# Kernel tuning notes

Measured on AMD Instinct MI355X. Metric: run time of the kernel, lower is better.

Reference implementation:

```python
import jax, jax.numpy as jnp
import numpy as np


def setup_inputs() -> dict:
    key = jax.random.key(0)
    k1, k2 = jax.random.split(key)
    B, P, H, W, D, C = 4, 8, 32, 32, 32, 16
    input_fmap = jax.random.normal(k1, (B, P, H, W, D, C), dtype=jnp.float32)
    # theta ~ identity affine (rows act on [y, x, z, 1]) + small noise so most
    # sampled coordinates fall inside the volume
    base = jnp.concatenate([jnp.eye(3, dtype=jnp.float32), jnp.zeros((3, 1), jnp.float32)], axis=1)
    theta = base[None, None] + 0.1 * jax.random.normal(k2, (B, P, 3, 4), dtype=jnp.float32)
    return {"input_fmap": input_fmap, "theta": theta}


def reference(input_fmap, theta):
    B, P, H, W, D, C = input_fmap.shape
    # --- affine grid generation (matches tf.meshgrid 'xy' indexing) ---
    xs = jnp.arange(W, dtype=jnp.float32)
    ys = jnp.arange(H, dtype=jnp.float32)
    zs = jnp.arange(D, dtype=jnp.float32)
    x_t, y_t, z_t = jnp.meshgrid(xs, ys, zs, indexing="xy")  # each (H, W, D)
    grid = jnp.stack([y_t.ravel(), x_t.ravel(), z_t.ravel(),
                      jnp.ones(H * W * D, jnp.float32)], axis=0)  # (4, HWD)
    batch_grids = jnp.einsum("bpij,jn->bpin", theta, grid)  # (B, P, 3, HWD)
    batch_grids = batch_grids.reshape(B, P, 3, H, W, D)
    y_s = batch_grids[:, :, 0]
    x_s = batch_grids[:, :, 1]
    z_s = batch_grids[:, :, 2]

    # --- trilinear sampling on a 2-voxel zero-padded volume ---
    fmap_p = jnp.pad(input_fmap, ((0, 0), (0, 0), (2, 2), (2, 2), (2, 2), (0, 0)))
    x = x_s + 2.0
    y = y_s + 2.0
    z = z_s + 2.0
    # NOTE: original code clips all three axes with H + 2 (faithful reproduction)
    hi = H + 2
    x0 = jnp.clip(jnp.floor(x).astype(jnp.int32), 0, hi)
    y0 = jnp.clip(jnp.floor(y).astype(jnp.int32), 0, hi)
    z0 = jnp.clip(jnp.floor(z).astype(jnp.int32), 0, hi)
    x1, y1, z1 = x0 + 1, y0 + 1, z0 + 1

    b_idx = jnp.arange(B)[:, None, None, None, None]
    p_idx = jnp.arange(P)[None, :, None, None, None]

    def gather(yy, xx, zz):
        # indices stacked as [y, x, z] in the original -> axes (H_pad, W_pad, D_pad)
        return fmap_p[b_idx, p_idx, yy, xx, zz]  # (B, P, H, W, D, C)

    c000 = gather(y0, x0, z0)
    c001 = gather(y0, x0, z1)
    c010 = gather(y1, x0, z0)
    c011 = gather(y1, x0, z1)
    c100 = gather(y0, x1, z0)
    c101 = gather(y0, x1, z1)
    c110 = gather(y1, x1, z0)
    c111 = gather(y1, x1, z1)

    xd = (x - x0.astype(jnp.float32))[..., None]
    yd = (y - y0.astype(jnp.float32))[..., None]
    zd = (z - z0.astype(jnp.float32))[..., None]

    out = (c000 * (1 - xd) * (1 - yd) * (1 - zd)
           + c100 * xd * (1 - yd) * (1 - zd)
           + c010 * (1 - xd) * yd * (1 - zd)
           + c001 * (1 - xd) * (1 - yd) * zd
           + c101 * xd * (1 - yd) * zd
           + c011 * (1 - xd) * yd * zd
           + c110 * xd * yd * (1 - zd)
           + c111 * xd * yd * zd)
    return out
```

## Files before the change

### kernel.cpp

```cpp
#include <hip/hip_runtime.h>

constexpr int B = 4, P = 8, H = 32, W = 32, D = 32, C = 16;

using f32x4 = __attribute__((ext_vector_type(4))) float;

__global__ __launch_bounds__(256) void resample3d_kernel(
    const float* __restrict__ fmap,
    const float* __restrict__ theta,
    float* __restrict__ out)
{
    const int bp  = blockIdx.x >> 9;
    const int tid = threadIdx.x;
    const int c4  = tid & 3;
    const int vox = blockIdx.x * 64 + (tid >> 2);
    const int k   =  vox        & (D - 1);
    const int j   = (vox >> 5)  & (W - 1);
    const int i   = (vox >> 10) & (H - 1);

    const float4* th4 = (const float4*)(theta + bp * 12);
    const float4 t0 = th4[0];
    const float4 t1 = th4[1];
    const float4 t2 = th4[2];

    const float fi = (float)i, fj = (float)j, fk = (float)k;
    const float y = fmaf(t0.x, fi, fmaf(t0.y, fj, fmaf(t0.z, fk, t0.w))) + 2.0f;
    const float x = fmaf(t1.x, fi, fmaf(t1.y, fj, fmaf(t1.z, fk, t1.w))) + 2.0f;
    const float z = fmaf(t2.x, fi, fmaf(t2.y, fj, fmaf(t2.z, fk, t2.w))) + 2.0f;

    const float fy0 = fminf(fmaxf(floorf(y), 0.0f), 34.0f);
    const float fx0 = fminf(fmaxf(floorf(x), 0.0f), 34.0f);
    const float fz0 = fminf(fmaxf(floorf(z), 0.0f), 34.0f);
    const float yd = y - fy0, xd = x - fx0, zd = z - fz0;

    const int ty0 = (int)fy0 - 2, tx0 = (int)fx0 - 2, tz0 = (int)fz0 - 2;

    float wy[2], wx[2], wz[2];
    int   iy[2], ix[2], iz[2];
    wy[0] = ((unsigned)ty0       < (unsigned)H) ? (1.0f - yd) : 0.0f;
    wy[1] = ((unsigned)(ty0 + 1) < (unsigned)H) ? yd          : 0.0f;
    wx[0] = ((unsigned)tx0       < (unsigned)W) ? (1.0f - xd) : 0.0f;
    wx[1] = ((unsigned)(tx0 + 1) < (unsigned)W) ? xd          : 0.0f;
    wz[0] = ((unsigned)tz0       < (unsigned)D) ? (1.0f - zd) : 0.0f;
    wz[1] = ((unsigned)(tz0 + 1) < (unsigned)D) ? zd          : 0.0f;
    iy[0] = min(max(ty0, 0), H - 1);  iy[1] = min(max(ty0 + 1, 0), H - 1);
    ix[0] = min(max(tx0, 0), W - 1);  ix[1] = min(max(tx0 + 1, 0), W - 1);
    iz[0] = min(max(tz0, 0), D - 1);  iz[1] = min(max(tz0 + 1, 0), D - 1);

    const float* base = fmap + bp * (H * W * D * C) + c4 * 4;

    f32x4 acc = {0.f, 0.f, 0.f, 0.f};
    #pragma unroll
    for (int a = 0; a < 2; ++a) {
        const int offy = iy[a] * (W * D * C);
        #pragma unroll
        for (int b2 = 0; b2 < 2; ++b2) {
            const int offyx = offy + ix[b2] * (D * C);
            const float wyx = wy[a] * wx[b2];
            #pragma unroll
            for (int c2 = 0; c2 < 2; ++c2) {
                const float w = wyx * wz[c2];
                const f32x4 v = *(const f32x4*)(base + offyx + iz[c2] * C);
                acc += w * v;
            }
        }
    }

    *(f32x4*)(out + vox * C + c4 * 4) = acc;
}

extern "C" void kernel_launch(void* const* d_in, const int* in_sizes, int n_in,
                              void* d_out, int out_size, void* d_ws, size_t ws_size,
                              hipStream_t stream) {
    const float* fmap  = (const float*)d_in[0];
    const float* theta = (const float*)d_in[1];
    float* out = (float*)d_out;

    const int total_threads = B * P * H * W * D * 4;
    const int block = 256;
    const int grid = total_threads / block;
    resample3d_kernel<<<grid, block, 0, stream>>>(fmap, theta, out);
}
```

Measured before the change: 29.14 us.

## Split z-corners across thread pairs, remap blocks across XCDs, nontemporal stores

Doubles the thread count so each pair of threads handles the two z-corners of a voxel. Each thread issues 4 gathers instead of 8, and the pair reduces its results with a cross-lane shuffle. Blocks are remapped so consecutive launch indices interleave across 8 groups, likely to spread each batch-patch volume across XCD L2 caches, and outputs use nontemporal stores. The cost is twice the index and weight arithmetic, the extra shuffles, and half the lanes staying idle at the store.

After: 29.71 us. Within noise of the previous version (+2.0%).

```diff
diff --git a/kernel.cpp b/kernel.cpp
--- a/kernel.cpp
+++ b/kernel.cpp
@@ -9,13 +9,17 @@
     const float* __restrict__ theta,
     float* __restrict__ out)
 {
-    const int bp  = blockIdx.x >> 9;
-    const int tid = threadIdx.x;
-    const int c4  = tid & 3;
-    const int vox = blockIdx.x * 64 + (tid >> 2);
+    const int orig = blockIdx.x;
+    const int virt = (orig & 7) * 4096 + (orig >> 3);
+
+    const int tid  = threadIdx.x;
+    const int zbit = (tid >> 2) & 1;
+    const int chunk = tid & 3;
+    const int vox = virt * 32 + (tid >> 3);
     const int k   =  vox        & (D - 1);
     const int j   = (vox >> 5)  & (W - 1);
     const int i   = (vox >> 10) & (H - 1);
+    const int bp  = virt >> 10;
 
     const float4* th4 = (const float4*)(theta + bp * 12);
     const float4 t0 = th4[0];
@@ -31,41 +35,48 @@
     const float fx0 = fminf(fmaxf(floorf(x), 0.0f), 34.0f);
     const float fz0 = fminf(fmaxf(floorf(z), 0.0f), 34.0f);
     const float yd = y - fy0, xd = x - fx0, zd = z - fz0;
-
     const int ty0 = (int)fy0 - 2, tx0 = (int)fx0 - 2, tz0 = (int)fz0 - 2;
 
-    float wy[2], wx[2], wz[2];
-    int   iy[2], ix[2], iz[2];
+    float wy[2], wx[2];
+    int   iy[2], ix[2];
     wy[0] = ((unsigned)ty0       < (unsigned)H) ? (1.0f - yd) : 0.0f;
     wy[1] = ((unsigned)(ty0 + 1) < (unsigned)H) ? yd          : 0.0f;
     wx[0] = ((unsigned)tx0       < (unsigned)W) ? (1.0f - xd) : 0.0f;
     wx[1] = ((unsigned)(tx0 + 1) < (unsigned)W) ? xd          : 0.0f;
-    wz[0] = ((unsigned)tz0       < (unsigned)D) ? (1.0f - zd) : 0.0f;
-    wz[1] = ((unsigned)(tz0 + 1) < (unsigned)D) ? zd          : 0.0f;
     iy[0] = min(max(ty0, 0), H - 1);  iy[1] = min(max(ty0 + 1, 0), H - 1);
     ix[0] = min(max(tx0, 0), W - 1);  ix[1] = min(max(tx0 + 1, 0), W - 1);
-    iz[0] = min(max(tz0, 0), D - 1);  iz[1] = min(max(tz0 + 1, 0), D - 1);
 
-    const float* base = fmap + bp * (H * W * D * C) + c4 * 4;
+    const int tz = tz0 + zbit;
+    const float wzl = ((unsigned)tz < (unsigned)D)
+                        ? (zbit ? zd : (1.0f - zd)) : 0.0f;
+    const int izl = min(max(tz, 0), D - 1);
+
+    const float* base = fmap + bp * (H * W * D * C) + izl * C + chunk * 4;
+
+    f32x4 v[4];
+    float w[4];
+    #pragma unroll
+    for (int a = 0; a < 2; ++a)
+        #pragma unroll
+        for (int b2 = 0; b2 < 2; ++b2) {
+            const int cn = a * 2 + b2;
+            w[cn] = wy[a] * wx[b2] * wzl;
+            v[cn] = *(const f32x4*)(base + iy[a] * (W * D * C) + ix[b2] * (D * C));
+        }
 
     f32x4 acc = {0.f, 0.f, 0.f, 0.f};
     #pragma unroll
-    for (int a = 0; a < 2; ++a) {
-        const int offy = iy[a] * (W * D * C);
-        #pragma unroll
-        for (int b2 = 0; b2 < 2; ++b2) {
-            const int offyx = offy + ix[b2] * (D * C);
-            const float wyx = wy[a] * wx[b2];
-            #pragma unroll
-            for (int c2 = 0; c2 < 2; ++c2) {
-                const float w = wyx * wz[c2];
-                const f32x4 v = *(const f32x4*)(base + offyx + iz[c2] * C);
-                acc += w * v;
-            }
-        }
+    for (int cn = 0; cn < 4; ++cn)
+        acc += w[cn] * v[cn];
+
+    #pragma unroll
+    for (int r = 0; r < 4; ++r)
+        acc[r] += __shfl_xor(acc[r], 4);
+
+    if (!zbit) {
+        float* outp = out + (size_t)vox * C + chunk * 4;
+        __builtin_nontemporal_store(acc, (f32x4*)outp);
     }
-
-    *(f32x4*)(out + vox * C + c4 * 4) = acc;
 }
 
 extern "C" void kernel_launch(void* const* d_in, const int* in_sizes, int n_in,
@@ -75,7 +86,7 @@
     const float* theta = (const float*)d_in[1];
     float* out = (float*)d_out;
 
-    const int total_threads = B * P * H * W * D * 4;
+    const int total_threads = B * P * H * W * D * 8;
     const int block = 256;
     const int grid = total_threads / block;
     resample3d_kernel<<<grid, block, 0, stream>>>(fmap, theta, out);
```

## Convert feature map to fp16 in workspace and gather with one thread per voxel

Applied to the files above, without the earlier changes.

Adds a pre-pass kernel that converts the fp32 input volume to fp16 in the workspace. A new gather kernel then reads the eight corners as half-precision vectors, one thread per voxel covering all 16 channels, and accumulates in fp16 before widening to fp32. It also swizzles block order across batch/patch volumes and uses nontemporal stores. The intent is to halve the bytes moved by the random gathers, at the cost of an extra full read and write pass over the input and reduced accuracy from fp16 weights and accumulation.

Result: slower. 66.13 us (+126.9%).

```diff
diff --git a/kernel.cpp b/kernel.cpp
--- a/kernel.cpp
+++ b/kernel.cpp
@@ -3,19 +3,33 @@
 constexpr int B = 4, P = 8, H = 32, W = 32, D = 32, C = 16;
 
 using f32x4 = __attribute__((ext_vector_type(4))) float;
+using f16x8 = __attribute__((ext_vector_type(8))) _Float16;
 
-__global__ __launch_bounds__(256) void resample3d_kernel(
-    const float* __restrict__ fmap,
+__global__ __launch_bounds__(256) void cvt_kernel(const float* __restrict__ in,
+                                                  _Float16* __restrict__ o) {
+    const int t = blockIdx.x * 256 + threadIdx.x;
+    const f32x4* p = (const f32x4*)in + (size_t)t * 2;
+    const f32x4 a = p[0], b = p[1];
+    f16x8 h;
+    h[0] = (_Float16)a[0]; h[1] = (_Float16)a[1];
+    h[2] = (_Float16)a[2]; h[3] = (_Float16)a[3];
+    h[4] = (_Float16)b[0]; h[5] = (_Float16)b[1];
+    h[6] = (_Float16)b[2]; h[7] = (_Float16)b[3];
+    *((f16x8*)o + t) = h;
+}
+
+__global__ __launch_bounds__(256) void gather_kernel(
+    const _Float16* __restrict__ fmap16,
     const float* __restrict__ theta,
     float* __restrict__ out)
 {
-    const int bp  = blockIdx.x >> 9;
-    const int tid = threadIdx.x;
-    const int c4  = tid & 3;
-    const int vox = blockIdx.x * 64 + (tid >> 2);
-    const int k   =  vox        & (D - 1);
-    const int j   = (vox >> 5)  & (W - 1);
-    const int i   = (vox >> 10) & (H - 1);
+    const int orig = blockIdx.x;
+    const int virt = (orig & 7) * 512 + (orig >> 3);
+    const int vox  = virt * 256 + threadIdx.x;
+    const int k = vox & (D - 1);
+    const int j = (vox >> 5) & (W - 1);
+    const int i = (vox >> 10) & (H - 1);
+    const int bp = vox >> 15;
 
     const float4* th4 = (const float4*)(theta + bp * 12);
     const float4 t0 = th4[0];
@@ -31,7 +45,94 @@
     const float fx0 = fminf(fmaxf(floorf(x), 0.0f), 34.0f);
     const float fz0 = fminf(fmaxf(floorf(z), 0.0f), 34.0f);
     const float yd = y - fy0, xd = x - fx0, zd = z - fz0;
+    const int ty0 = (int)fy0 - 2, tx0 = (int)fx0 - 2, tz0 = (int)fz0 - 2;
 
+    float wy[2], wx[2], wz[2];
+    int   iy[2], ix[2], iz[2];
+    wy[0] = ((unsigned)ty0       < (unsigned)H) ? (1.0f - yd) : 0.0f;
+    wy[1] = ((unsigned)(ty0 + 1) < (unsigned)H) ? yd          : 0.0f;
+    wx[0] = ((unsigned)tx0       < (unsigned)W) ? (1.0f - xd) : 0.0f;
+    wx[1] = ((unsigned)(tx0 + 1) < (unsigned)W) ? xd          : 0.0f;
+    wz[0] = ((unsigned)tz0       < (unsigned)D) ? (1.0f - zd) : 0.0f;
+    wz[1] = ((unsigned)(tz0 + 1) < (unsigned)D) ? zd          : 0.0f;
+    iy[0] = min(max(ty0, 0), H - 1);  iy[1] = min(max(ty0 + 1, 0), H - 1);
+    ix[0] = min(max(tx0, 0), W - 1);  ix[1] = min(max(tx0 + 1, 0), W - 1);
+    iz[0] = min(max(tz0, 0), D - 1);  iz[1] = min(max(tz0 + 1, 0), D - 1);
+
+    int   off[8];
+    float w[8];
+    #pragma unroll
+    for (int a = 0; a < 2; ++a)
+        #pragma unroll
+        for (int b2 = 0; b2 < 2; ++b2)
+            #pragma unroll
+            for (int c2 = 0; c2 < 2; ++c2) {
+                const int cn = a * 4 + b2 * 2 + c2;
+                off[cn] = ((iy[a] * W + ix[b2]) * D + iz[c2]) * C;
+                w[cn]   = wy[a] * wx[b2] * wz[c2];
+            }
+
+    const _Float16* base = fmap16 + (size_t)bp * (H * W * D * C);
+
+    f16x8 v0[8], v1[8];
+    #pragma unroll
+    for (int cn = 0; cn < 8; ++cn) {
+        v0[cn] = *(const f16x8*)(base + off[cn]);
+        v1[cn] = *(const f16x8*)(base + off[cn] + 8);
+    }
+
+    f16x8 aA0 = 0, aA1 = 0, aB0 = 0, aB1 = 0;
+    #pragma unroll
+    for (int cn = 0; cn < 4; ++cn) {
+        const _Float16 hw = (_Float16)w[cn];
+        aA0 += hw * v0[cn];
+        aA1 += hw * v1[cn];
+    }
+    #pragma unroll
+    for (int cn = 4; cn < 8; ++cn) {
+        const _Float16 hw = (_Float16)w[cn];
+        aB0 += hw * v0[cn];
+        aB1 += hw * v1[cn];
+    }
+
+    float r[16];
+    #pragma unroll
+    for (int c = 0; c < 8; ++c) {
+        r[c]     = (float)aA0[c] + (float)aB0[c];
+        r[c + 8] = (float)aA1[c] + (float)aB1[c];
+    }
+
+    float* op = out + (size_t)vox * C;
+    __builtin_nontemporal_store(*(f32x4*)&r[0],  (f32x4*)op);
+    __builtin_nontemporal_store(*(f32x4*)&r[4],  (f32x4*)(op + 4));
+    __builtin_nontemporal_store(*(f32x4*)&r[8],  (f32x4*)(op + 8));
+    __builtin_nontemporal_store(*(f32x4*)&r[12], (f32x4*)(op + 12));
+}
+
+__global__ __launch_bounds__(256) void fallback_kernel(
+    const float* __restrict__ fmap, const float* __restrict__ theta,
+    float* __restrict__ out)
+{
+    const int bp  = blockIdx.x >> 9;
+    const int tid = threadIdx.x;
+    const int c4  = tid & 3;
+    const int vox = blockIdx.x * 64 + (tid >> 2);
+    const int k   =  vox        & (D - 1);
+    const int j   = (vox >> 5)  & (W - 1);
+    const int i   = (vox >> 10) & (H - 1);
+
+    const float4* th4 = (const float4*)(theta + bp * 12);
+    const float4 t0 = th4[0], t1 = th4[1], t2 = th4[2];
+
+    const float fi = (float)i, fj = (float)j, fk = (float)k;
+    const float y = fmaf(t0.x, fi, fmaf(t0.y, fj, fmaf(t0.z, fk, t0.w))) + 2.0f;
+    const float x = fmaf(t1.x, fi, fmaf(t1.y, fj, fmaf(t1.z, fk, t1.w))) + 2.0f;
+    const float z = fmaf(t2.x, fi, fmaf(t2.y, fj, fmaf(t2.z, fk, t2.w))) + 2.0f;
+
+    const float fy0 = fminf(fmaxf(floorf(y), 0.0f), 34.0f);
+    const float fx0 = fminf(fmaxf(floorf(x), 0.0f), 34.0f);
+    const float fz0 = fminf(fmaxf(floorf(z), 0.0f), 34.0f);
+    const float yd = y - fy0, xd = x - fx0, zd = z - fz0;
     const int ty0 = (int)fy0 - 2, tx0 = (int)fx0 - 2, tz0 = (int)fz0 - 2;
 
     float wy[2], wx[2], wz[2];
@@ -47,25 +148,19 @@
     iz[0] = min(max(tz0, 0), D - 1);  iz[1] = min(max(tz0 + 1, 0), D - 1);
 
     const float* base = fmap + bp * (H * W * D * C) + c4 * 4;
-
     f32x4 acc = {0.f, 0.f, 0.f, 0.f};
     #pragma unroll
-    for (int a = 0; a < 2; ++a) {
-        const int offy = iy[a] * (W * D * C);
+    for (int a = 0; a < 2; ++a)
         #pragma unroll
-        for (int b2 = 0; b2 < 2; ++b2) {
-            const int offyx = offy + ix[b2] * (D * C);
-            const float wyx = wy[a] * wx[b2];
+        for (int b2 = 0; b2 < 2; ++b2)
             #pragma unroll
             for (int c2 = 0; c2 < 2; ++c2) {
-                const float w = wyx * wz[c2];
-                const f32x4 v = *(const f32x4*)(base + offyx + iz[c2] * C);
-                acc += w * v;
+                const float wgt = wy[a] * wx[b2] * wz[c2];
+                const f32x4 v = *(const f32x4*)(
+                    base + ((iy[a] * W + ix[b2]) * D + iz[c2]) * C);
+                acc += wgt * v;
             }
-        }
-    }
-
-    *(f32x4*)(out + vox * C + c4 * 4) = acc;
+    *(f32x4*)(out + (size_t)vox * C + c4 * 4) = acc;
 }
 
 extern "C" void kernel_launch(void* const* d_in, const int* in_sizes, int n_in,
@@ -75,8 +170,15 @@
     const float* theta = (const float*)d_in[1];
     float* out = (float*)d_out;
 
-    const int total_threads = B * P * H * W * D * 4;
-    const int block = 256;
-    const int grid = total_threads / block;
-    resample3d_kernel<<<grid, block, 0, stream>>>(fmap, theta, out);
+    const size_t need = (size_t)(B * P * H * W * D * C) * sizeof(_Float16);
+    if (ws_size >= need) {
+        _Float16* f16buf = (_Float16*)d_ws;
+        const int cvt_blocks = (B * P * H * W * D * C / 8) / 256;
+        cvt_kernel<<<cvt_blocks, 256, 0, stream>>>(fmap, f16buf);
+        const int gat_blocks = (B * P * H * W * D) / 256;
+        gather_kernel<<<gat_blocks, 256, 0, stream>>>(f16buf, theta, out);
+    } else {
+        const int total_threads = B * P * H * W * D * 4;
+        fallback_kernel<<<total_threads / 256, 256, 0, stream>>>(fmap, theta, out);
+    }
 }
```

## Stage per-tile source bounding box in LDS as fp16 and interpolate from shared memory

Applied to the files above, without the earlier changes.

Each block now handles an 8x8x8 output tile. It computes the affine bounding box of the source voxels the tile needs and, when that box fits in capacity, loads the box into LDS converted to fp16. The eight trilinear taps are then read from shared memory and accumulated with packed fp16 math. Blocks are also remapped so that neighbouring block IDs cover different tiles, and a global-memory fp32 fallback remains for large boxes. The aim is to cut redundant global gathers, at the cost of fp16 precision loss in both the staged values and the accumulation, plus extra LDS use that limits occupancy.

Result: slower. 59.01 us (+102.5%).

```diff
diff --git a/kernel.cpp b/kernel.cpp
--- a/kernel.cpp
+++ b/kernel.cpp
@@ -2,70 +2,178 @@
 
 constexpr int B = 4, P = 8, H = 32, W = 32, D = 32, C = 16;
 
+constexpr int TI = 8, TJ = 8, TK = 8;
+constexpr int TILE_VOX = TI * TJ * TK;
+constexpr int CAP = 2048;
+
 using f32x4 = __attribute__((ext_vector_type(4))) float;
+using f16x4 = __attribute__((ext_vector_type(4))) _Float16;
+using f16x8 = __attribute__((ext_vector_type(8))) _Float16;
 
-__global__ __launch_bounds__(256) void resample3d_kernel(
+__global__ __launch_bounds__(256) void resample_tile(
     const float* __restrict__ fmap,
     const float* __restrict__ theta,
     float* __restrict__ out)
 {
-    const int bp  = blockIdx.x >> 9;
-    const int tid = threadIdx.x;
-    const int c4  = tid & 3;
-    const int vox = blockIdx.x * 64 + (tid >> 2);
-    const int k   =  vox        & (D - 1);
-    const int j   = (vox >> 5)  & (W - 1);
-    const int i   = (vox >> 10) & (H - 1);
+    extern __shared__ _Float16 sm[];
+
+    const int orig = blockIdx.x;
+    const int virt = (orig & 7) * 256 + (orig >> 3);
+    const int bp = virt >> 6;
+    const int t6 = virt & 63;
+    const int i0 = (t6 >> 4) * TI;
+    const int j0 = ((t6 >> 2) & 3) * TJ;
+    const int k0 = (t6 & 3) * TK;
 
     const float4* th4 = (const float4*)(theta + bp * 12);
     const float4 t0 = th4[0];
     const float4 t1 = th4[1];
     const float4 t2 = th4[2];
 
-    const float fi = (float)i, fj = (float)j, fk = (float)k;
-    const float y = fmaf(t0.x, fi, fmaf(t0.y, fj, fmaf(t0.z, fk, t0.w))) + 2.0f;
-    const float x = fmaf(t1.x, fi, fmaf(t1.y, fj, fmaf(t1.z, fk, t1.w))) + 2.0f;
-    const float z = fmaf(t2.x, fi, fmaf(t2.y, fj, fmaf(t2.z, fk, t2.w))) + 2.0f;
+    const float fi0 = (float)i0, fj0 = (float)j0, fk0 = (float)k0;
+    const float pyb = fmaf(t0.x, fi0, fmaf(t0.y, fj0, fmaf(t0.z, fk0, t0.w))) + 2.0f;
+    const float pxb = fmaf(t1.x, fi0, fmaf(t1.y, fj0, fmaf(t1.z, fk0, t1.w))) + 2.0f;
+    const float pzb = fmaf(t2.x, fi0, fmaf(t2.y, fj0, fmaf(t2.z, fk0, t2.w))) + 2.0f;
 
-    const float fy0 = fminf(fmaxf(floorf(y), 0.0f), 34.0f);
-    const float fx0 = fminf(fmaxf(floorf(x), 0.0f), 34.0f);
-    const float fz0 = fminf(fmaxf(floorf(z), 0.0f), 34.0f);
-    const float yd = y - fy0, xd = x - fx0, zd = z - fz0;
+    const float eyi = t0.x * (TI - 1), eyj = t0.y * (TJ - 1), eyk = t0.z * (TK - 1);
+    const float exi = t1.x * (TI - 1), exj = t1.y * (TJ - 1), exk = t1.z * (TK - 1);
+    const float ezi = t2.x * (TI - 1), ezj = t2.y * (TJ - 1), ezk = t2.z * (TK - 1);
 
-    const int ty0 = (int)fy0 - 2, tx0 = (int)fx0 - 2, tz0 = (int)fz0 - 2;
+    const float pymin = pyb + fminf(eyi, 0.f) + fminf(eyj, 0.f) + fminf(eyk, 0.f);
+    const float pymax = pyb + fmaxf(eyi, 0.f) + fmaxf(eyj, 0.f) + fmaxf(eyk, 0.f);
+    const float pxmin = pxb + fminf(exi, 0.f) + fminf(exj, 0.f) + fminf(exk, 0.f);
+    const float pxmax = pxb + fmaxf(exi, 0.f) + fmaxf(exj, 0.f) + fmaxf(exk, 0.f);
+    const float pzmin = pzb + fminf(ezi, 0.f) + fminf(ezj, 0.f) + fminf(ezk, 0.f);
+    const float pzmax = pzb + fmaxf(ezi, 0.f) + fmaxf(ezj, 0.f) + fmaxf(ezk, 0.f);
 
-    float wy[2], wx[2], wz[2];
-    int   iy[2], ix[2], iz[2];
-    wy[0] = ((unsigned)ty0       < (unsigned)H) ? (1.0f - yd) : 0.0f;
-    wy[1] = ((unsigned)(ty0 + 1) < (unsigned)H) ? yd          : 0.0f;
-    wx[0] = ((unsigned)tx0       < (unsigned)W) ? (1.0f - xd) : 0.0f;
-    wx[1] = ((unsigned)(tx0 + 1) < (unsigned)W) ? xd          : 0.0f;
-    wz[0] = ((unsigned)tz0       < (unsigned)D) ? (1.0f - zd) : 0.0f;
-    wz[1] = ((unsigned)(tz0 + 1) < (unsigned)D) ? zd          : 0.0f;
-    iy[0] = min(max(ty0, 0), H - 1);  iy[1] = min(max(ty0 + 1, 0), H - 1);
-    ix[0] = min(max(tx0, 0), W - 1);  ix[1] = min(max(tx0 + 1, 0), W - 1);
-    iz[0] = min(max(tz0, 0), D - 1);  iz[1] = min(max(tz0 + 1, 0), D - 1);
+    const int tylo = max(0, min((int)fminf(fmaxf(floorf(pymin), 0.f), 34.f) - 2, 31));
+    int       tyhi = min(31, (int)fminf(fmaxf(floorf(pymax), 0.f), 34.f) - 1);
+    tyhi = max(tyhi, tylo);
+    const int txlo = max(0, min((int)fminf(fmaxf(floorf(pxmin), 0.f), 34.f) - 2, 31));
+    int       txhi = min(31, (int)fminf(fmaxf(floorf(pxmax), 0.f), 34.f) - 1);
+    txhi = max(txhi, txlo);
+    const int tzlo = max(0, min((int)fminf(fmaxf(floorf(pzmin), 0.f), 34.f) - 2, 31));
+    int       tzhi = min(31, (int)fminf(fmaxf(floorf(pzmax), 0.f), 34.f) - 1);
+    tzhi = max(tzhi, tzlo);
 
-    const float* base = fmap + bp * (H * W * D * C) + c4 * 4;
+    const int dy = tyhi - tylo + 1;
+    const int dx = txhi - txlo + 1;
+    const int dz = tzhi - tzlo + 1;
+    const int vol = dy * dx * dz;
+    const bool fast = (vol <= CAP);
 
-    f32x4 acc = {0.f, 0.f, 0.f, 0.f};
-    #pragma unroll
-    for (int a = 0; a < 2; ++a) {
-        const int offy = iy[a] * (W * D * C);
-        #pragma unroll
-        for (int b2 = 0; b2 < 2; ++b2) {
-            const int offyx = offy + ix[b2] * (D * C);
-            const float wyx = wy[a] * wx[b2];
-            #pragma unroll
-            for (int c2 = 0; c2 < 2; ++c2) {
-                const float w = wyx * wz[c2];
-                const f32x4 v = *(const f32x4*)(base + offyx + iz[c2] * C);
-                acc += w * v;
+    const float* slice = fmap + bp * (H * W * D * C);
+
+    if (fast) {
+        const int wv = threadIdx.x >> 6;
+        const int ln = threadIdx.x & 63;
+        const int rowch = dz * 4;
+        int ry = 0, rx = wv;
+        while (rx >= dx) { rx -= dx; ++ry; }
+        while (ry < dy) {
+            const float* g = slice + ((tylo + ry) * W + (txlo + rx)) * (D * C)
+                                   + tzlo * C;
+            _Float16* l = sm + ((ry * dx + rx) * dz) * 16;
+            for (int cz = ln; cz < rowch; cz += 64) {
+                const f32x4 v = *(const f32x4*)(g + cz * 4);
+                f16x4 h;
+                h[0] = (_Float16)v[0]; h[1] = (_Float16)v[1];
+                h[2] = (_Float16)v[2]; h[3] = (_Float16)v[3];
+                *(f16x4*)(l + cz * 4) = h;
             }
+            rx += 4;
+            while (rx >= dx) { rx -= dx; ++ry; }
         }
     }
+    __syncthreads();
 
-    *(f32x4*)(out + vox * C + c4 * 4) = acc;
+    for (int v = threadIdx.x; v < TILE_VOX; v += 256) {
+        const int li = v >> 6;
+        const int lj = (v >> 3) & 7;
+        const int lk = v & 7;
+        const float fi = (float)(i0 + li), fj = (float)(j0 + lj), fk = (float)(k0 + lk);
+
+        const float py = fmaf(t0.x, fi, fmaf(t0.y, fj, fmaf(t0.z, fk, t0.w))) + 2.0f;
+        const float px = fmaf(t1.x, fi, fmaf(t1.y, fj, fmaf(t1.z, fk, t1.w))) + 2.0f;
+        const float pz = fmaf(t2.x, fi, fmaf(t2.y, fj, fmaf(t2.z, fk, t2.w))) + 2.0f;
+
+        const float fy0 = fminf(fmaxf(floorf(py), 0.f), 34.f);
+        const float fx0 = fminf(fmaxf(floorf(px), 0.f), 34.f);
+        const float fz0 = fminf(fmaxf(floorf(pz), 0.f), 34.f);
+        const float yd = py - fy0, xd = px - fx0, zd = pz - fz0;
+        const int ty0 = (int)fy0 - 2, tx0 = (int)fx0 - 2, tz0 = (int)fz0 - 2;
+
+        float wy[2], wx[2], wz[2];
+        int   iy[2], ix[2], iz[2];
+        wy[0] = ((unsigned)ty0       < (unsigned)H) ? (1.0f - yd) : 0.0f;
+        wy[1] = ((unsigned)(ty0 + 1) < (unsigned)H) ? yd          : 0.0f;
+        wx[0] = ((unsigned)tx0       < (unsigned)W) ? (1.0f - xd) : 0.0f;
+        wx[1] = ((unsigned)(tx0 + 1) < (unsigned)W) ? xd          : 0.0f;
+        wz[0] = ((unsigned)tz0       < (unsigned)D) ? (1.0f - zd) : 0.0f;
+        wz[1] = ((unsigned)(tz0 + 1) < (unsigned)D) ? zd          : 0.0f;
+        iy[0] = min(max(ty0, 0), H - 1);  iy[1] = min(max(ty0 + 1, 0), H - 1);
+        ix[0] = min(max(tx0, 0), W - 1);  ix[1] = min(max(tx0 + 1, 0), W - 1);
+        iz[0] = min(max(tz0, 0), D - 1);  iz[1] = min(max(tz0 + 1, 0), D - 1);
+
+        f32x4 r0, r1, r2, r3;
+
+        if (fast) {
+            int ly[2], lx[2], lz[2];
+            ly[0] = min(max(iy[0] - tylo, 0), dy - 1);
+            ly[1] = min(max(iy[1] - tylo, 0), dy - 1);
+            lx[0] = min(max(ix[0] - txlo, 0), dx - 1);
+            lx[1] = min(max(ix[1] - txlo, 0), dx - 1);
+            lz[0] = min(max(iz[0] - tzlo, 0), dz - 1);
+            lz[1] = min(max(iz[1] - tzlo, 0), dz - 1);
+
+            f16x8 aA0 = 0, aA1 = 0, aB0 = 0, aB1 = 0;
+            #pragma unroll
+            for (int a = 0; a < 2; ++a)
+                #pragma unroll
+                for (int b2 = 0; b2 < 2; ++b2)
+                    #pragma unroll
+                    for (int c2 = 0; c2 < 2; ++c2) {
+                        const int cn = a * 4 + b2 * 2 + c2;
+                        const int vx = ((ly[a] * dx + lx[b2]) * dz + lz[c2]) * 16;
+                        const f16x8 lo = *(const f16x8*)(sm + vx);
+                        const f16x8 hi = *(const f16x8*)(sm + vx + 8);
+                        const _Float16 h = (_Float16)(wy[a] * wx[b2] * wz[c2]);
+                        const f16x8 h8 = {h, h, h, h, h, h, h, h};
+                        if (cn < 4) { aA0 += h8 * lo; aA1 += h8 * hi; }
+                        else        { aB0 += h8 * lo; aB1 += h8 * hi; }
+                    }
+            #pragma unroll
+            for (int c = 0; c < 4; ++c) {
+                r0[c] = (float)aA0[c]     + (float)aB0[c];
+                r1[c] = (float)aA0[c + 4] + (float)aB0[c + 4];
+                r2[c] = (float)aA1[c]     + (float)aB1[c];
+                r3[c] = (float)aA1[c + 4] + (float)aB1[c + 4];
+            }
+        } else {
+            f32x4 acc[4] = {{0,0,0,0},{0,0,0,0},{0,0,0,0},{0,0,0,0}};
+            #pragma unroll
+            for (int a = 0; a < 2; ++a)
+                #pragma unroll
+                for (int b2 = 0; b2 < 2; ++b2)
+                    #pragma unroll
+                    for (int c2 = 0; c2 < 2; ++c2) {
+                        const float wgt = wy[a] * wx[b2] * wz[c2];
+                        const float* p = slice +
+                            ((iy[a] * W + ix[b2]) * D + iz[c2]) * C;
+                        #pragma unroll
+                        for (int q = 0; q < 4; ++q)
+                            acc[q] += wgt * *(const f32x4*)(p + q * 4);
+                    }
+            r0 = acc[0]; r1 = acc[1]; r2 = acc[2]; r3 = acc[3];
+        }
+
+        float* op = out + ((bp * H + (i0 + li)) * W + (j0 + lj)) * (D * C)
+                        + (k0 + lk) * C;
+        *(f32x4*)(op)      = r0;
+        *(f32x4*)(op + 4)  = r1;
+        *(f32x4*)(op + 8)  = r2;
+        *(f32x4*)(op + 12) = r3;
+    }
 }
 
 extern "C" void kernel_launch(void* const* d_in, const int* in_sizes, int n_in,
@@ -75,8 +183,7 @@
     const float* theta = (const float*)d_in[1];
     float* out = (float*)d_out;
 
-    const int total_threads = B * P * H * W * D * 4;
-    const int block = 256;
-    const int grid = total_threads / block;
-    resample3d_kernel<<<grid, block, 0, stream>>>(fmap, theta, out);
+    const int grid = (B * P * H * W * D) / TILE_VOX;
+    const size_t lds = (size_t)CAP * C * sizeof(_Float16);
+    resample_tile<<<grid, 256, lds, stream>>>(fmap, theta, out);
 }
```
